# Optimization experiments

Measured on AMD Instinct MI355X. Metric: run time of the kernel, lower is better.

Reference implementation:

```python
import jax, jax.numpy as jnp
import numpy as np

BN_EPS = 1e-5


def setup_inputs() -> dict:
    key = jax.random.key(0)
    ks = jax.random.split(key, 4)
    N, C, T, V, S = 64, 64, 300, 25, 3
    x = jax.random.normal(ks[0], (N, C, T, V), dtype=jnp.float32)
    PA = jax.random.uniform(ks[1], (S, V, V), dtype=jnp.float32)
    # 1x1 conv weights per subset, branch-init scale sqrt(2/(out*1*1*branches))
    Wc = jax.random.normal(ks[2], (S, C, C), dtype=jnp.float32) * np.sqrt(2.0 / (C * S))
    bc = jnp.zeros((S, C), dtype=jnp.float32)
    gamma = jnp.ones((C,), dtype=jnp.float32)
    beta = jnp.zeros((C,), dtype=jnp.float32)
    return {"x": x, "PA": PA, "Wc": Wc, "bc": bc, "gamma": gamma, "beta": beta}


def reference(x, PA, Wc, bc, gamma, beta):
    # x: [N,C,T,V]; PA: [S,V,V]; Wc: [S,Cout,Cin]; bc: [S,Cout]
    # L2_norm: per-column L2 norm along dim=1 of each subset adjacency
    A = PA / (jnp.linalg.norm(PA, axis=1, keepdims=True) + 1e-4)  # [S,V,V]
    # For each subset: (x.view(N,CT,V) @ A[s]) then 1x1 conv, summed over subsets.
    # out[n,o,t,w] = sum_s sum_c sum_v x[n,c,t,v] * A[s,v,w] * Wc[s,o,c] + sum_s bc[s,o]
    y = jnp.einsum('nctv,svw,soc->notw', x, A, Wc)
    y = y + bc.sum(axis=0)[None, :, None, None]
    # BatchNorm2d (training-mode batch statistics) over (N,T,V) per channel
    mean = y.mean(axis=(0, 2, 3), keepdims=True)
    var = y.var(axis=(0, 2, 3), keepdims=True)
    y = (y - mean) * jax.lax.rsqrt(var + BN_EPS)
    y = y * gamma[None, :, None, None] + beta[None, :, None, None]
    # residual (identity since in_channels == out_channels) + ReLU
    return jax.nn.relu(y + x)
```

## Files before the change

kernel.cpp:

```cpp
#include <hip/hip_runtime.h>
#include <hip/hip_bf16.h>
#include <math.h>

typedef __attribute__((ext_vector_type(8))) short short8v;
typedef __attribute__((ext_vector_type(4))) float f32x4;

#define NB 64
#define CC 64
#define TT 300
#define VV 25
#define SS 3
#define TB 4
#define TBLK (TT/TB)

#define AFA_BYTES 36864
#define WCF_BYTES 49152
#define YOFF_BYTES 131072

static __device__ __forceinline__ unsigned short f2bf(float f){
    union { __hip_bfloat16 h; unsigned short s; } u;
    u.h = __float2bfloat16(f);
    return u.s;
}
static __device__ __forceinline__ float bf2f(unsigned short b){
    return __uint_as_float(((unsigned)b) << 16);
}
static __device__ __forceinline__ void pack2(const f32x4& z, unsigned& d0, unsigned& d1){
    d0 = (unsigned)f2bf(z[0]) | ((unsigned)f2bf(z[1]) << 16);
    d1 = (unsigned)f2bf(z[2]) | ((unsigned)f2bf(z[3]) << 16);
}
static __device__ __forceinline__ short8v mk8(unsigned q0,unsigned q1,unsigned q2,unsigned q3){
    union { unsigned u[4]; short8v v; } x;
    x.u[0]=q0; x.u[1]=q1; x.u[2]=q2; x.u[3]=q3;
    return x.v;
}

__global__ void gcn_prep(const float* __restrict__ PA, const float* __restrict__ Wc,
                         float* __restrict__ ws)
{
    __shared__ float inv[SS][VV];
    const int tid = threadIdx.x;
    const int nz = 8192 / 8;
    for (int i = tid; i < nz; i += 384) ws[blockIdx.x * nz + i] = 0.f;
    if (blockIdx.x != 0) return;

    if (tid < SS*VV){
        int s = tid/VV, w = tid%VV;
        float sum = 0.f;
        for (int v=0; v<VV; ++v){ float p = PA[s*VV*VV + v*VV + w]; sum = fmaf(p,p,sum); }
        inv[s][w] = 1.f/(sqrtf(sum)+1e-4f);
    }
    __syncthreads();
    {
        int s = tid/128, rem = tid%128, nt = rem/64, lane = rem%64;
        int w = nt*16 + (lane&15), g = lane>>4;
        short8v vals;
        #pragma unroll
        for (int j=0;j<8;++j){
            int v = 8*g + j;
            float f = (v<VV && w<VV) ? PA[s*VV*VV + v*VV + w]*inv[s][w] : 0.f;
            vals[j] = (short)f2bf(f);
        }
        *(short8v*)((char*)ws + AFA_BYTES + (size_t)((s*2+nt)*64 + lane)*16) = vals;
    }
    for (int fid = tid; fid < SS*4*2*64; fid += 384){
        int lane = fid & 63;
        int kt = (fid >> 6) & 1;
        int ot = (fid >> 7) & 3;
        int s  = fid >> 9;
        int o  = 16*ot + (lane & 15);
        int c0 = kt*32 + 8*(lane >> 4);
        short8v vals;
        #pragma unroll
        for (int j=0;j<8;++j) vals[j] = (short)f2bf(Wc[((size_t)s*CC + o)*CC + c0 + j]);
        *(short8v*)((char*)ws + WCF_BYTES + (size_t)fid*16) = vals;
    }
}

template<bool YB>
__global__ __launch_bounds__(256,4) void gcn_main_kernel(
    const float* __restrict__ x, float* __restrict__ ws,
    float* __restrict__ yf32, __hip_bfloat16* __restrict__ ybf)
{
    __shared__ __align__(16) unsigned short lds[CC*100];

    const int tid  = threadIdx.x;
    const int lane = tid & 63;
    const int wv   = tid >> 6;
    const int l15  = lane & 15, g = lane >> 4;
    const int n    = blockIdx.x / TBLK;
    const int t0   = (blockIdx.x % TBLK) * TB;
    const int t    = t0 + wv;

    short8v axf[4];
    #pragma unroll
    for (int mt=0; mt<4; ++mt){
        const int c = 16*mt + l15;
        const float* p = x + ((size_t)(n*CC + c)*TT + t)*VV + 8*g;
        short8v f;
        if (g < 3){
            float4 a = *(const float4*)p;
            float4 b = *(const float4*)(p+4);
            f[0]=(short)f2bf(a.x); f[1]=(short)f2bf(a.y); f[2]=(short)f2bf(a.z); f[3]=(short)f2bf(a.w);
            f[4]=(short)f2bf(b.x); f[5]=(short)f2bf(b.y); f[6]=(short)f2bf(b.z); f[7]=(short)f2bf(b.w);
        } else {
            f[0]=(short)f2bf(p[0]);
            f[1]=0; f[2]=0; f[3]=0; f[4]=0; f[5]=0; f[6]=0; f[7]=0;
        }
        axf[mt] = f;
    }

    const short8v* afrag = (const short8v*)((const char*)ws + AFA_BYTES);
    const short8v* wfrag = (const short8v*)((const char*)ws + WCF_BYTES);

    const f32x4 zf = {0.f,0.f,0.f,0.f};
    f32x4 yacc[4][2];
    #pragma unroll
    for (int ot=0; ot<4; ++ot){ yacc[ot][0]=zf; yacc[ot][1]=zf; }

    const int sLo = 32*(g&1) + l15;
    const int sHi = sLo + 16;
    const bool hi = (lane >= 32);

    #pragma unroll 1
    for (int s=0; s<SS; ++s){
        short8v aA0 = afrag[(s*2+0)*64 + lane];
        short8v aA1 = afrag[(s*2+1)*64 + lane];
        #pragma unroll
        for (int kt=0; kt<2; ++kt){
            f32x4 z00 = __builtin_amdgcn_mfma_f32_16x16x32_bf16(axf[2*kt+0], aA0, zf, 0,0,0);
            f32x4 z01 = __builtin_amdgcn_mfma_f32_16x16x32_bf16(axf[2*kt+0], aA1, zf, 0,0,0);
            f32x4 z10 = __builtin_amdgcn_mfma_f32_16x16x32_bf16(axf[2*kt+1], aA0, zf, 0,0,0);
            f32x4 z11 = __builtin_amdgcn_mfma_f32_16x16x32_bf16(axf[2*kt+1], aA1, zf, 0,0,0);
            unsigned pLo0n0, pLo1n0, pLo0n1, pLo1n1;
            unsigned pHi0n0, pHi1n0, pHi0n1, pHi1n1;
            pack2(z00, pLo0n0, pLo1n0);
            pack2(z01, pLo0n1, pLo1n1);
            pack2(z10, pHi0n0, pHi1n0);
            pack2(z11, pHi0n1, pHi1n1);
            unsigned a0,b0,a1,b1,a2,b2,a3,b3;
            a0=__shfl(pLo0n0,sLo); b0=__shfl(pHi0n0,sLo);
            a1=__shfl(pLo1n0,sLo); b1=__shfl(pHi1n0,sLo);
            a2=__shfl(pLo0n0,sHi); b2=__shfl(pHi0n0,sHi);
            a3=__shfl(pLo1n0,sHi); b3=__shfl(pHi1n0,sHi);
            short8v bz0 = mk8(hi?b0:a0, hi?b1:a1, hi?b2:a2, hi?b3:a3);
            a0=__shfl(pLo0n1,sLo); b0=__shfl(pHi0n1,sLo);
            a1=__shfl(pLo1n1,sLo); b1=__shfl(pHi1n1,sLo);
            a2=__shfl(pLo0n1,sHi); b2=__shfl(pHi0n1,sHi);
            a3=__shfl(pLo1n1,sHi); b3=__shfl(pHi1n1,sHi);
            short8v bz1 = mk8(hi?b0:a0, hi?b1:a1, hi?b2:a2, hi?b3:a3);
            #pragma unroll
            for (int ot=0; ot<4; ++ot){
                short8v wc = wfrag[((s*4+ot)*2+kt)*64 + lane];
                yacc[ot][0] = __builtin_amdgcn_mfma_f32_16x16x32_bf16(wc, bz0, yacc[ot][0], 0,0,0);
                yacc[ot][1] = __builtin_amdgcn_mfma_f32_16x16x32_bf16(wc, bz1, yacc[ot][1], 0,0,0);
            }
        }
    }

    #pragma unroll
    for (int ot=0; ot<4; ++ot){
        #pragma unroll
        for (int r=0; r<4; ++r){
            const int o = 16*ot + 4*g + r;
            lds[o*100 + wv*25 + l15] = f2bf(yacc[ot][0][r]);
            if (l15 < VV-16)
                lds[o*100 + wv*25 + 16 + l15] = f2bf(yacc[ot][1][r]);
        }
    }
    __syncthreads();

    for (int i = tid; i < 1600; i += 256){
        const int row = i / 25;
        const int c8  = i % 25;
        uint2 d = *(const uint2*)&lds[row*100 + c8*4];
        const size_t base = (size_t)(n*CC + row)*(TT*VV) + (size_t)t0*VV + c8*4;
        if (YB){
            *(uint2*)((unsigned short*)ybf + base) = d;
        } else {
            float4 f;
            f.x = bf2f((unsigned short)(d.x & 0xffff));
            f.y = bf2f((unsigned short)(d.x >> 16));
            f.z = bf2f((unsigned short)(d.y & 0xffff));
            f.w = bf2f((unsigned short)(d.y >> 16));
            *(float4*)(yf32 + base) = f;
        }
    }

    {
        const int o = tid >> 2, q = tid & 3;
        float s1 = 0.f, s2 = 0.f;
        for (int gr = q; gr < 25; gr += 4){
            uint2 d = *(const uint2*)&lds[o*100 + gr*4];
            float a0 = bf2f((unsigned short)(d.x & 0xffff));
            float a1 = bf2f((unsigned short)(d.x >> 16));
            float a2 = bf2f((unsigned short)(d.y & 0xffff));
            float a3 = bf2f((unsigned short)(d.y >> 16));
            s1 += (a0+a1)+(a2+a3);
            s2 = fmaf(a0,a0,fmaf(a1,a1,fmaf(a2,a2,fmaf(a3,a3,s2))));
        }
        s1 += __shfl_xor(s1,1); s1 += __shfl_xor(s1,2);
        s2 += __shfl_xor(s2,1); s2 += __shfl_xor(s2,2);
        if (q == 0){
            atomicAdd(&ws[n*128 + o],      s1);
            atomicAdd(&ws[n*128 + 64 + o], s2);
        }
    }
}

__global__ void gcn_finalize_kernel(const float* __restrict__ gamma,
                                    const float* __restrict__ beta,
                                    float* __restrict__ ws)
{
    const int o = threadIdx.x;
    if (o < CC) {
        float s = 0.f, q = 0.f;
        for (int n = 0; n < NB; ++n){
            s += ws[n*128 + o];
            q += ws[n*128 + 64 + o];
        }
        const float cnt = (float)(NB * TT * VV);
        const float mean = s / cnt;
        const float var  = q / cnt - mean * mean;
        const float sc   = gamma[o] * rsqrtf(var + 1e-5f);
        ws[8192 + o] = sc;
        ws[8256 + o] = beta[o] - mean * sc;
    }
}

template<bool YB>
__global__ __launch_bounds__(256) void gcn_bn_relu_kernel(
    const float* __restrict__ x, float* __restrict__ out,
    const float* __restrict__ ws, const unsigned short* __restrict__ ybf)
{
    const int total4 = NB * CC * TT * VV / 4;
    const int per_c4 = TT * VV / 4;
    for (int i = blockIdx.x * 256 + threadIdx.x; i < total4; i += gridDim.x * 256) {
        const int c = (i / per_c4) & (CC - 1);
        const float sc = ws[8192 + c];
        const float sh = ws[8256 + c];
        float4 yv;
        if (YB){
            uint2 yb = *(const uint2*)&ybf[4*i];
            yv.x = bf2f((unsigned short)(yb.x & 0xffff));
            yv.y = bf2f((unsigned short)(yb.x >> 16));
            yv.z = bf2f((unsigned short)(yb.y & 0xffff));
            yv.w = bf2f((unsigned short)(yb.y >> 16));
        } else {
            yv = reinterpret_cast<float4*>(out)[i];
        }
        float4 xv = reinterpret_cast<const float4*>(x)[i];
        float4 r;
        r.x = fmaxf(fmaf(yv.x, sc, sh) + xv.x, 0.f);
        r.y = fmaxf(fmaf(yv.y, sc, sh) + xv.y, 0.f);
        r.z = fmaxf(fmaf(yv.z, sc, sh) + xv.z, 0.f);
        r.w = fmaxf(fmaf(yv.w, sc, sh) + xv.w, 0.f);
        reinterpret_cast<float4*>(out)[i] = r;
    }
}

extern "C" void kernel_launch(void* const* d_in, const int* in_sizes, int n_in,
                              void* d_out, int out_size, void* d_ws, size_t ws_size,
                              hipStream_t stream)
{
    const float* x     = (const float*)d_in[0];
    const float* PA    = (const float*)d_in[1];
    const float* Wc    = (const float*)d_in[2];
    const float* gamma = (const float*)d_in[4];
    const float* beta  = (const float*)d_in[5];
    float* out = (float*)d_out;
    float* ws  = (float*)d_ws;

    const size_t ybytes = (size_t)NB*CC*TT*VV*2;
    const bool yb = ws_size >= (size_t)YOFF_BYTES + ybytes;
    __hip_bfloat16* ybf = (__hip_bfloat16*)((char*)d_ws + YOFF_BYTES);

    gcn_prep<<<8, 384, 0, stream>>>(PA, Wc, ws);
    if (yb){
        gcn_main_kernel<true><<<NB*TBLK, 256, 0, stream>>>(x, ws, out, ybf);
        gcn_finalize_kernel<<<1, 64, 0, stream>>>(gamma, beta, ws);
        gcn_bn_relu_kernel<true><<<2048, 256, 0, stream>>>(x, out, ws, (const unsigned short*)ybf);
    } else {
        gcn_main_kernel<false><<<NB*TBLK, 256, 0, stream>>>(x, ws, out, ybf);
        gcn_finalize_kernel<<<1, 64, 0, stream>>>(gamma, beta, ws);
        gcn_bn_relu_kernel<false><<<2048, 256, 0, stream>>>(x, out, ws, (const unsigned short*)ybf);
    }
}
```

Before: 125.5 us.

## Fuse main, finalize and BN-ReLU into one persistent cooperative kernel

Adds a cooperative persistent kernel that zeroes the statistics buffer, loops over time tiles computing the graph convolution, and accumulates per-channel sums. It then grid-syncs, reduces the statistics per block into LDS, and applies BN, residual and ReLU in the same launch. The goal is to remove the separate finalize and elementwise kernel launches and their inter-kernel gaps. Each block also prefetches the next tile's input into registers while computing the current one. This adds two grid-wide barriers and caps the grid at occupancy times CU count. If the cooperative launch fails, it falls back to the old three-kernel path.

Measured after the change: 288.1 us. 2.3x slower.

```diff
diff --git a/kernel.cpp b/kernel.cpp
--- a/kernel.cpp
+++ b/kernel.cpp
@@ -1,6 +1,9 @@
 #include <hip/hip_runtime.h>
 #include <hip/hip_bf16.h>
+#include <hip/hip_cooperative_groups.h>
 #include <math.h>
+
+namespace cg = cooperative_groups;
 
 typedef __attribute__((ext_vector_type(8))) short short8v;
 typedef __attribute__((ext_vector_type(4))) float f32x4;
@@ -12,6 +15,10 @@
 #define SS 3
 #define TB 4
 #define TBLK (TT/TB)
+#define TILES (NB*TBLK)
+#define TOTAL4 (NB*CC*TT*VV/4)
+#define PERC4  (TT*VV/4)
+#define CNTF   480000.0f
 
 #define AFA_BYTES 36864
 #define WCF_BYTES 49152
@@ -33,6 +40,201 @@
     union { unsigned u[4]; short8v v; } x;
     x.u[0]=q0; x.u[1]=q1; x.u[2]=q2; x.u[3]=q3;
     return x.v;
+}
+
+static __device__ __forceinline__ void gatherx(const float* __restrict__ x,
+                                               int n, int t, int l15, int g, float4* ra)
+{
+    #pragma unroll
+    for (int mt=0; mt<4; ++mt){
+        const int c = 16*mt + l15;
+        const float* p = x + ((size_t)(n*CC + c)*TT + t)*VV + 8*g;
+        if (g < 3){
+            ra[2*mt]   = *(const float4*)p;
+            ra[2*mt+1] = *(const float4*)(p+4);
+        } else {
+            ra[2*mt].x = p[0];
+        }
+    }
+}
+static __device__ __forceinline__ void cvtx(const float4* ra, int g, short8v* axf)
+{
+    #pragma unroll
+    for (int mt=0; mt<4; ++mt){
+        short8v f;
+        if (g < 3){
+            float4 a = ra[2*mt], b = ra[2*mt+1];
+            f[0]=(short)f2bf(a.x); f[1]=(short)f2bf(a.y); f[2]=(short)f2bf(a.z); f[3]=(short)f2bf(a.w);
+            f[4]=(short)f2bf(b.x); f[5]=(short)f2bf(b.y); f[6]=(short)f2bf(b.z); f[7]=(short)f2bf(b.w);
+        } else {
+            f[0]=(short)f2bf(ra[2*mt].x);
+            f[1]=0; f[2]=0; f[3]=0; f[4]=0; f[5]=0; f[6]=0; f[7]=0;
+        }
+        axf[mt] = f;
+    }
+}
+
+__global__ __launch_bounds__(256,4) void gcn_fused(
+    const float* __restrict__ x, float* __restrict__ ws,
+    float* __restrict__ out, const float* __restrict__ gamma,
+    const float* __restrict__ beta, __hip_bfloat16* __restrict__ ybf)
+{
+    __shared__ __align__(16) unsigned short lds[CC*100];
+    float* lf = (float*)lds;
+    cg::grid_group gridg = cg::this_grid();
+
+    const int tid  = threadIdx.x;
+    const int lane = tid & 63;
+    const int wv   = tid >> 6;
+    const int l15  = lane & 15, g = lane >> 4;
+
+    for (int i = blockIdx.x*256 + tid; i < 8192; i += gridDim.x*256) ws[i] = 0.f;
+    if (blockIdx.x == 0){
+    }
+    gridg.sync();
+
+    const short8v* afrag = (const short8v*)((const char*)ws + AFA_BYTES);
+    const short8v* wfrag = (const short8v*)((const char*)ws + WCF_BYTES);
+    const f32x4 zf = {0.f,0.f,0.f,0.f};
+    const int sLo = 32*(g&1) + l15;
+    const int sHi = sLo + 16;
+    const bool hi = (lane >= 32);
+
+    float4 ra[8];
+    int tile = blockIdx.x;
+    if (tile < TILES){
+        gatherx(x, tile/TBLK, (tile%TBLK)*TB + wv, l15, g, ra);
+    }
+    for (; tile < TILES; tile += gridDim.x){
+        const int n  = tile / TBLK;
+        const int t0 = (tile % TBLK) * TB;
+
+        short8v axf[4];
+        cvtx(ra, g, axf);
+        const int nxt = tile + gridDim.x;
+        if (nxt < TILES)
+            gatherx(x, nxt/TBLK, (nxt%TBLK)*TB + wv, l15, g, ra);
+
+        f32x4 yacc[4][2];
+        #pragma unroll
+        for (int ot=0; ot<4; ++ot){ yacc[ot][0]=zf; yacc[ot][1]=zf; }
+
+        #pragma unroll 1
+        for (int s=0; s<SS; ++s){
+            short8v aA0 = afrag[(s*2+0)*64 + lane];
+            short8v aA1 = afrag[(s*2+1)*64 + lane];
+            #pragma unroll
+            for (int kt=0; kt<2; ++kt){
+                f32x4 z00 = __builtin_amdgcn_mfma_f32_16x16x32_bf16(axf[2*kt+0], aA0, zf, 0,0,0);
+                f32x4 z01 = __builtin_amdgcn_mfma_f32_16x16x32_bf16(axf[2*kt+0], aA1, zf, 0,0,0);
+                f32x4 z10 = __builtin_amdgcn_mfma_f32_16x16x32_bf16(axf[2*kt+1], aA0, zf, 0,0,0);
+                f32x4 z11 = __builtin_amdgcn_mfma_f32_16x16x32_bf16(axf[2*kt+1], aA1, zf, 0,0,0);
+                unsigned pLo0n0, pLo1n0, pLo0n1, pLo1n1;
+                unsigned pHi0n0, pHi1n0, pHi0n1, pHi1n1;
+                pack2(z00, pLo0n0, pLo1n0);
+                pack2(z01, pLo0n1, pLo1n1);
+                pack2(z10, pHi0n0, pHi1n0);
+                pack2(z11, pHi0n1, pHi1n1);
+                unsigned a0,b0,a1,b1,a2,b2,a3,b3;
+                a0=__shfl(pLo0n0,sLo); b0=__shfl(pHi0n0,sLo);
+                a1=__shfl(pLo1n0,sLo); b1=__shfl(pHi1n0,sLo);
+                a2=__shfl(pLo0n0,sHi); b2=__shfl(pHi0n0,sHi);
+                a3=__shfl(pLo1n0,sHi); b3=__shfl(pHi1n0,sHi);
+                short8v bz0 = mk8(hi?b0:a0, hi?b1:a1, hi?b2:a2, hi?b3:a3);
+                a0=__shfl(pLo0n1,sLo); b0=__shfl(pHi0n1,sLo);
+                a1=__shfl(pLo1n1,sLo); b1=__shfl(pHi1n1,sLo);
+                a2=__shfl(pLo0n1,sHi); b2=__shfl(pHi0n1,sHi);
+                a3=__shfl(pLo1n1,sHi); b3=__shfl(pHi1n1,sHi);
+                short8v bz1 = mk8(hi?b0:a0, hi?b1:a1, hi?b2:a2, hi?b3:a3);
+                #pragma unroll
+                for (int ot=0; ot<4; ++ot){
+                    short8v wc = wfrag[((s*4+ot)*2+kt)*64 + lane];
+                    yacc[ot][0] = __builtin_amdgcn_mfma_f32_16x16x32_bf16(wc, bz0, yacc[ot][0], 0,0,0);
+                    yacc[ot][1] = __builtin_amdgcn_mfma_f32_16x16x32_bf16(wc, bz1, yacc[ot][1], 0,0,0);
+                }
+            }
+        }
+
+        __syncthreads();
+        #pragma unroll
+        for (int ot=0; ot<4; ++ot){
+            #pragma unroll
+            for (int r=0; r<4; ++r){
+                const int o = 16*ot + 4*g + r;
+                lds[o*100 + wv*25 + l15] = f2bf(yacc[ot][0][r]);
+                if (l15 < VV-16)
+                    lds[o*100 + wv*25 + 16 + l15] = f2bf(yacc[ot][1][r]);
+            }
+        }
+        __syncthreads();
+
+        for (int i = tid; i < 1600; i += 256){
+            const int row = i / 25;
+            const int c8  = i % 25;
+            uint2 d = *(const uint2*)&lds[row*100 + c8*4];
+            const size_t base = (size_t)(n*CC + row)*(TT*VV) + (size_t)t0*VV + c8*4;
+            *(uint2*)((unsigned short*)ybf + base) = d;
+        }
+        {
+            const int o = tid >> 2, q = tid & 3;
+            float s1 = 0.f, s2 = 0.f;
+            for (int gr = q; gr < 25; gr += 4){
+                uint2 d = *(const uint2*)&lds[o*100 + gr*4];
+                float a0 = bf2f((unsigned short)(d.x & 0xffff));
+                float a1 = bf2f((unsigned short)(d.x >> 16));
+                float a2 = bf2f((unsigned short)(d.y & 0xffff));
+                float a3 = bf2f((unsigned short)(d.y >> 16));
+                s1 += (a0+a1)+(a2+a3);
+                s2 = fmaf(a0,a0,fmaf(a1,a1,fmaf(a2,a2,fmaf(a3,a3,s2))));
+            }
+            s1 += __shfl_xor(s1,1); s1 += __shfl_xor(s1,2);
+            s2 += __shfl_xor(s2,1); s2 += __shfl_xor(s2,2);
+            if (q == 0){
+                atomicAdd(&ws[n*128 + o],      s1);
+                atomicAdd(&ws[n*128 + 64 + o], s2);
+            }
+        }
+    }
+    gridg.sync();
+
+    {
+        const int o = tid >> 2, q = tid & 3;
+        float s = 0.f, sq = 0.f;
+        for (int nn = q*16; nn < q*16 + 16; ++nn){
+            s  += ws[nn*128 + o];
+            sq += ws[nn*128 + 64 + o];
+        }
+        s  += __shfl_xor(s,1);  s  += __shfl_xor(s,2);
+        sq += __shfl_xor(sq,1); sq += __shfl_xor(sq,2);
+        __syncthreads();
+        if (q == 0){
+            const float mean = s / CNTF;
+            const float var  = sq / CNTF - mean*mean;
+            const float sc   = gamma[o] * rsqrtf(var + 1e-5f);
+            lf[o]      = sc;
+            lf[64 + o] = beta[o] - mean*sc;
+        }
+        __syncthreads();
+    }
+
+    for (int i = blockIdx.x*256 + tid; i < TOTAL4; i += gridDim.x*256){
+        const int c = (i / PERC4) & (CC - 1);
+        const float sc = lf[c];
+        const float sh = lf[64 + c];
+        uint2 yb = *(const uint2*)&((const unsigned short*)ybf)[4*i];
+        float4 yv;
+        yv.x = bf2f((unsigned short)(yb.x & 0xffff));
+        yv.y = bf2f((unsigned short)(yb.x >> 16));
+        yv.z = bf2f((unsigned short)(yb.y & 0xffff));
+        yv.w = bf2f((unsigned short)(yb.y >> 16));
+        float4 xv = reinterpret_cast<const float4*>(x)[i];
+        float4 r;
+        r.x = fmaxf(fmaf(yv.x, sc, sh) + xv.x, 0.f);
+        r.y = fmaxf(fmaf(yv.y, sc, sh) + xv.y, 0.f);
+        r.z = fmaxf(fmaf(yv.z, sc, sh) + xv.z, 0.f);
+        r.w = fmaxf(fmaf(yv.w, sc, sh) + xv.w, 0.f);
+        reinterpret_cast<float4*>(out)[i] = r;
+    }
 }
 
 __global__ void gcn_prep(const float* __restrict__ PA, const float* __restrict__ Wc,
@@ -92,23 +294,10 @@
     const int t0   = (blockIdx.x % TBLK) * TB;
     const int t    = t0 + wv;
 
+    float4 ra[8];
+    gatherx(x, n, t, l15, g, ra);
     short8v axf[4];
-    #pragma unroll
-    for (int mt=0; mt<4; ++mt){
-        const int c = 16*mt + l15;
-        const float* p = x + ((size_t)(n*CC + c)*TT + t)*VV + 8*g;
-        short8v f;
-        if (g < 3){
-            float4 a = *(const float4*)p;
-            float4 b = *(const float4*)(p+4);
-            f[0]=(short)f2bf(a.x); f[1]=(short)f2bf(a.y); f[2]=(short)f2bf(a.z); f[3]=(short)f2bf(a.w);
-            f[4]=(short)f2bf(b.x); f[5]=(short)f2bf(b.y); f[6]=(short)f2bf(b.z); f[7]=(short)f2bf(b.w);
-        } else {
-            f[0]=(short)f2bf(p[0]);
-            f[1]=0; f[2]=0; f[3]=0; f[4]=0; f[5]=0; f[6]=0; f[7]=0;
-        }
-        axf[mt] = f;
-    }
+    cvtx(ra, g, axf);
 
     const short8v* afrag = (const short8v*)((const char*)ws + AFA_BYTES);
     const short8v* wfrag = (const short8v*)((const char*)ws + WCF_BYTES);
@@ -186,7 +375,6 @@
             *(float4*)(yf32 + base) = f;
         }
     }
-
     {
         const int o = tid >> 2, q = tid & 3;
         float s1 = 0.f, s2 = 0.f;
@@ -219,9 +407,8 @@
             s += ws[n*128 + o];
             q += ws[n*128 + 64 + o];
         }
-        const float cnt = (float)(NB * TT * VV);
-        const float mean = s / cnt;
-        const float var  = q / cnt - mean * mean;
+        const float mean = s / CNTF;
+        const float var  = q / CNTF - mean * mean;
         const float sc   = gamma[o] * rsqrtf(var + 1e-5f);
         ws[8192 + o] = sc;
         ws[8256 + o] = beta[o] - mean * sc;
@@ -233,10 +420,8 @@
     const float* __restrict__ x, float* __restrict__ out,
     const float* __restrict__ ws, const unsigned short* __restrict__ ybf)
 {
-    const int total4 = NB * CC * TT * VV / 4;
-    const int per_c4 = TT * VV / 4;
-    for (int i = blockIdx.x * 256 + threadIdx.x; i < total4; i += gridDim.x * 256) {
-        const int c = (i / per_c4) & (CC - 1);
+    for (int i = blockIdx.x * 256 + threadIdx.x; i < TOTAL4; i += gridDim.x * 256) {
+        const int c = (i / PERC4) & (CC - 1);
         const float sc = ws[8192 + c];
         const float sh = ws[8256 + c];
         float4 yv;
@@ -276,12 +461,26 @@
     __hip_bfloat16* ybf = (__hip_bfloat16*)((char*)d_ws + YOFF_BYTES);
 
     gcn_prep<<<8, 384, 0, stream>>>(PA, Wc, ws);
+
     if (yb){
-        gcn_main_kernel<true><<<NB*TBLK, 256, 0, stream>>>(x, ws, out, ybf);
+        int occ = 0, nCU = 0, dev = 0;
+        hipGetDevice(&dev);
+        hipDeviceGetAttribute(&nCU, hipDeviceAttributeMultiprocessorCount, dev);
+        hipError_t oe = hipOccupancyMaxActiveBlocksPerMultiprocessor(&occ, gcn_fused, 256, 0);
+        if (oe == hipSuccess && occ >= 1 && nCU >= 1){
+            int grid = occ * nCU;
+            if (grid > TILES) grid = TILES;
+            void* args[] = {(void*)&x, (void*)&ws, (void*)&out,
+                            (void*)&gamma, (void*)&beta, (void*)&ybf};
+            hipError_t rc = hipLaunchCooperativeKernel(gcn_fused, dim3(grid), dim3(256),
+                                                       args, 0, stream);
+            if (rc == hipSuccess) return;
+        }
+        gcn_main_kernel<true><<<TILES, 256, 0, stream>>>(x, ws, out, ybf);
         gcn_finalize_kernel<<<1, 64, 0, stream>>>(gamma, beta, ws);
         gcn_bn_relu_kernel<true><<<2048, 256, 0, stream>>>(x, out, ws, (const unsigned short*)ybf);
     } else {
-        gcn_main_kernel<false><<<NB*TBLK, 256, 0, stream>>>(x, ws, out, ybf);
+        gcn_main_kernel<false><<<TILES, 256, 0, stream>>>(x, ws, out, ybf);
         gcn_finalize_kernel<<<1, 64, 0, stream>>>(gamma, beta, ws);
         gcn_bn_relu_kernel<false><<<2048, 256, 0, stream>>>(x, out, ws, (const unsigned short*)ybf);
     }
```
